# Kernel tuning notes

Measured on AMD Instinct MI355X. Metric: run time of the kernel, lower is better.

## Reference

```python
import jax, jax.numpy as jnp
import numpy as np


def _refl_conv(x, w, b, pad, stride):
    # ReflectionPad2d(pad) followed by Conv2d(stride=stride), NCHW / OIHW layouts.
    x = jnp.pad(x, ((0, 0), (0, 0), (pad, pad), (pad, pad)), mode='reflect')
    y = jax.lax.conv_general_dilated(
        x, w, window_strides=(stride, stride), padding='VALID',
        dimension_numbers=('NCHW', 'OIHW', 'NCHW'))
    return y + b[None, :, None, None]


def setup_inputs() -> dict:
    key = jax.random.key(0)
    ks = jax.random.split(key, 16)
    B, C, H, W = 8, 128, 64, 64
    IH, IW = 4 * H, 4 * W
    g = 0.02  # init gain ('normal' init in source)
    f32 = jnp.float32
    return {
        'feature_in': jax.random.normal(ks[0], (B, C, H, W), f32),
        'imgs': jax.random.uniform(ks[1], (B, 3, IH, IW), dtype=f32),
        'masks': jax.random.uniform(ks[2], (B, 1, IH, IW), dtype=f32),
        # Gate conv stack params (torch OIHW layout), biases zero per init_weights
        'gw1': g * jax.random.normal(ks[3], (32, 4, 7, 7), f32),
        'gb1': jnp.zeros((32,), f32),
        'gw2': g * jax.random.normal(ks[4], (64, 32, 5, 5), f32),
        'gb2': jnp.zeros((64,), f32),
        'gw3': g * jax.random.normal(ks[5], (128, 64, 5, 5), f32),
        'gb3': jnp.zeros((128,), f32),
        'gw4': g * jax.random.normal(ks[6], (256, 128, 3, 3), f32),
        'gb4': jnp.zeros((256,), f32),
        'gw5': g * jax.random.normal(ks[7], (1, 256, 3, 3), f32),
        'gb5': jnp.zeros((1,), f32),
        # combiner: Conv2d(2C -> C, 1x1)
        'cw': g * jax.random.normal(ks[8], (C, 2 * C, 1, 1), f32),
        'cb': jnp.zeros((C,), f32),
    }


def reference(feature_in, imgs, masks, gw1, gb1, gw2, gb2, gw3, gb3,
              gw4, gb4, gw5, gb5, cw, cb):
    PI = 3.1415926
    # ---- Gate ----
    x = jnp.concatenate([imgs, masks], axis=1)          # [B,4,4H,4W]
    s = jax.nn.relu(_refl_conv(x, gw1, gb1, 3, 1))
    s = jax.nn.relu(_refl_conv(s, gw2, gb2, 2, 2))
    s = jax.nn.relu(_refl_conv(s, gw3, gb3, 2, 1))
    s = jax.nn.relu(_refl_conv(s, gw4, gb4, 1, 2))
    s = jax.nn.relu(_refl_conv(s, gw5, gb5, 1, 1))      # [B,1,H,W]
    s = jnp.tan(PI * (jnp.tanh(s) - 0.5))
    B, C, H, W = feature_in.shape
    P = H * W
    gate = s.reshape(B, P, 1, 1)                        # row-major pixel order
    # ---- Att (patch_size=1: kernels are per-pixel feature vectors) ----
    K = feature_in.reshape(B, C, P).transpose(0, 2, 1) + 1e-7   # [B,P,C]
    Kn = K / jnp.sqrt(jnp.sum(K * K, axis=-1, keepdims=True))
    # attention_scores = conv2d(feature_map, K_norm) == cosine-like similarity
    scores = jnp.einsum('bpc,bcyx->bpyx', Kn, feature_in) + gate  # [B,P,H,W]
    A = jax.nn.softmax(scores, axis=1)
    # conv_transpose2d with 1x1 kernels == weighted sum of (unnormalized) kernels
    att = jnp.einsum('bpyx,bpc->bcyx', A, K)            # [B,C,H,W]
    # ---- combiner (1x1 conv on concat) ----
    cat = jnp.concatenate([att, feature_in], axis=1)    # [B,2C,H,W]
    out = jnp.einsum('oc,bcyx->boyx', cw[:, :, 0, 0], cat) + cb[None, :, None, None]
    return out
```

## Files before the change

### kernel.cpp

```cpp
#include <hip/hip_runtime.h>
#include <hip/hip_bf16.h>
#include <hip/hip_fp16.h>
#include <math.h>


#define PI_F 3.1415926f

typedef __attribute__((ext_vector_type(8))) short short8;
typedef __attribute__((ext_vector_type(4))) float f32x4;
typedef _Float16 half8 __attribute__((ext_vector_type(8)));
typedef __attribute__((ext_vector_type(4))) unsigned short u16x4;
typedef unsigned short ushort_t;

__device__ __forceinline__ ushort_t f2bf(float x) {
    unsigned u = __float_as_uint(x);
    unsigned r = (u + 0x7FFFu + ((u >> 16) & 1u)) >> 16;
    return (ushort_t)r;
}
__device__ __forceinline__ void split16(float x, ushort_t& h, ushort_t& l) {
    __half hh = __float2half(x);
    h = __half_as_ushort(hh);
    l = __half_as_ushort(__float2half(x - __half2float(hh)));
}
__device__ __forceinline__ ushort_t f2h(float x) {
    return __half_as_ushort(__float2half(x));
}
__device__ __forceinline__ int swz(int r, int c) {
    return ((c ^ r ^ (r >> 2)) & 3) << 3;
}

__global__ __launch_bounds__(256) void transform_w_k(
    const float* __restrict__ w, ushort_t* __restrict__ Wh, ushort_t* __restrict__ Wl,
    int Cout, int Cin, int KK)
{
    int idx = blockIdx.x * 256 + threadIdx.x;
    int N = Cout * Cin * KK;
    if (idx >= N) return;
    int oc = idx / (Cin * KK);
    int rem = idx - oc * (Cin * KK);
    int ic = rem / KK;
    int t = rem - ic * KK;
    float v = w[idx];
    long dst = ((long)t * Cout + oc) * Cin + ic;
    split16(v, Wh[dst], Wl[dst]);
}

__global__ __launch_bounds__(256) void transform_w1_k(
    const float* __restrict__ w, ushort_t* __restrict__ Wh, ushort_t* __restrict__ Wl)
{
    int idx = blockIdx.x * 256 + threadIdx.x;
    if (idx >= 7 * 32 * 32) return;
    int ky = idx / 1024;
    int rem = idx - ky * 1024;
    int oc = rem >> 5;
    int k = rem & 31;
    float v = 0.f;
    if (k < 28) {
        int kx = k >> 2, ic = k & 3;
        v = w[((oc * 4 + ic) * 7 + ky) * 7 + kx];
    }
    split16(v, Wh[idx], Wl[idx]);
}

__global__ __launch_bounds__(256) void prep_in_k(
    const float* __restrict__ imgs, const float* __restrict__ masks,
    ushort_t* __restrict__ Xh)
{
    const int iy = blockIdx.x, b = blockIdx.y;
    int sy = iy - 3; if (sy < 0) sy = -sy; if (sy >= 256) sy = 510 - sy;
    const int rb = sy << 8;
    const float* i0 = imgs + (long)b * 3 * 65536;
    const float* mk = masks + (long)b * 65536;
    for (int x = threadIdx.x; x < 262; x += 256) {
        int sx = x - 3; if (sx < 0) sx = -sx; if (sx >= 256) sx = 510 - sx;
        u16x4 hv;
        hv[0] = f2h(i0[rb + sx]);
        hv[1] = f2h(i0[65536 + rb + sx]);
        hv[2] = f2h(i0[131072 + rb + sx]);
        hv[3] = f2h(mk[rb + sx]);
        long o = ((long)(b * 262 + iy) * 262 + x) * 4;
        *(u16x4*)&Xh[o] = hv;
    }
}

__global__ __launch_bounds__(256) void conv1_mfma_k(
    const ushort_t* __restrict__ Xinh,
    const ushort_t* __restrict__ W1h, const ushort_t* __restrict__ W1l,
    const float* __restrict__ bias, ushort_t* __restrict__ Oh)
{
    const int tid = threadIdx.x, lane = tid & 63, wid = tid >> 6;
    const int wm = wid & 1, wn = wid >> 1, l15 = lane & 15, quad = lane >> 4;
    const int ox0 = blockIdx.x * 64;
    const int oy = blockIdx.y, b = blockIdx.z;
    f32x4 acc[2];
    acc[0] = (f32x4){0.f, 0.f, 0.f, 0.f};
    acc[1] = (f32x4){0.f, 0.f, 0.f, 0.f};
#pragma unroll
    for (int ky = 0; ky < 7; ++ky) {
        long wo = (long)(ky * 32 + wm * 16 + l15) * 32 + quad * 8;
        half8 Ah = *(const half8*)&W1h[wo];
        half8 Al = *(const half8*)&W1l[wo];
        long xrow = ((long)(b * 262 + oy + ky) * 262 + ox0) * 4;
#pragma unroll
        for (int ni = 0; ni < 2; ++ni) {
            long xo = xrow + (wn * 32 + ni * 16 + l15) * 4 + quad * 8;
            half8 Bh = *(const half8*)&Xinh[xo];
            acc[ni] = __builtin_amdgcn_mfma_f32_16x16x32_f16(Ah, Bh, acc[ni], 0, 0, 0);
            acc[ni] = __builtin_amdgcn_mfma_f32_16x16x32_f16(Al, Bh, acc[ni], 0, 0, 0);
        }
    }
    const int ocf = wm * 16 + quad * 4;
    float4 bv = *(const float4*)&bias[ocf];
#pragma unroll
    for (int ni = 0; ni < 2; ++ni) {
        int n = ox0 + wn * 32 + ni * 16 + l15;
        u16x4 hv;
        hv[0] = f2h(fmaxf(acc[ni][0] + bv.x, 0.f));
        hv[1] = f2h(fmaxf(acc[ni][1] + bv.y, 0.f));
        hv[2] = f2h(fmaxf(acc[ni][2] + bv.z, 0.f));
        hv[3] = f2h(fmaxf(acc[ni][3] + bv.w, 0.f));
        long o = ((long)(b * 260 + oy + 2) * 260 + n + 2) * 32 + ocf;
        *(u16x4*)&Oh[o] = hv;
    }
}

__global__ __launch_bounds__(256) void pad_cl_k(
    ushort_t* __restrict__ Xh, int Hp, int Wp, int PAD, int C, int H, int W)
{
    const int iy = blockIdx.x, b = blockIdx.y;
    int t = iy - PAD; if (t < 0) t = -t; if (t >= H) t = 2 * H - 2 - t;
    const int iys = t + PAD;
    const long rowd = ((long)(b * Hp + iy) * Wp) * C;
    const long rows = ((long)(b * Hp + iys) * Wp) * C;
    const int nch = Wp * (C >> 3);
    for (int idx = threadIdx.x; idx < nch; idx += 256) {
        int x = idx / (C >> 3);
        int cg = (idx - x * (C >> 3)) << 3;
        int t2 = x - PAD; if (t2 < 0) t2 = -t2; if (t2 >= W) t2 = 2 * W - 2 - t2;
        int xs = t2 + PAD;
        if (xs == x && iys == iy) continue;
        *(int4*)&Xh[rowd + (long)x * C + cg] = *(const int4*)&Xh[rows + (long)xs * C + cg];
    }
}

template<int K, int S, int CIN, int CSTG, int MT, int NPX, bool WRITE_CL>
__global__ __launch_bounds__(256, 2) void conv_mfma_k(
    const ushort_t* __restrict__ Xh,
    const ushort_t* __restrict__ Wh, const ushort_t* __restrict__ Wl,
    const float* __restrict__ bias,
    int Hp, int Wp, int CoutT,
    ushort_t* __restrict__ Oh, int Hpn, int Wpn, int NP,
    float* __restrict__ Ofp)
{
    constexpr int WS = (NPX - 1) * S + K;
    constexpr int WS2 = (WS + 1) / 2;
    constexpr int MF = MT / 32;
    constexpr int NF = NPX / 32;
    __shared__ ushort_t Bsh[WS * CSTG];
    __shared__ ushort_t Ash[K * MT * CSTG];
    __shared__ ushort_t Asl[K * MT * CSTG];
    const int tid = threadIdx.x, lane = tid & 63, wid = tid >> 6;
    const int wm = wid & 1, wn = wid >> 1, l15 = lane & 15, quad = lane >> 4;
    const int bx = blockIdx.x, oy = blockIdx.y;
    const int NOC = CoutT / MT;
    const int ocg = blockIdx.z % NOC, b = blockIdx.z / NOC;
    const int ox0 = bx * NPX;

    f32x4 acc[MF][NF];
#pragma unroll
    for (int mi = 0; mi < MF; ++mi)
#pragma unroll
        for (int ni = 0; ni < NF; ++ni) acc[mi][ni] = (f32x4){0.f, 0.f, 0.f, 0.f};

#pragma unroll
    for (int ky = 0; ky < K; ++ky) {
        const long rowoff = ((long)(b * Hp + oy * S + ky) * Wp + ox0 * S) * CIN;
        for (int cs = 0; cs < CIN; cs += CSTG) {
            __syncthreads();
            constexpr int NCH = WS * CSTG / 8;
#pragma unroll
            for (int it = 0; it < (NCH + 255) / 256; ++it) {
                int flat = tid + it * 256;
                if (flat < NCH) {
                    int e0 = flat * 8;
                    int x = e0 / CSTG;
                    int cpos = (e0 - x * CSTG) >> 3;
                    int xs = (S == 1) ? x : ((x >> 1) + (x & 1) * WS2);
                    *(int4*)&Bsh[xs * CSTG + swz(xs, cpos)] =
                        *(const int4*)&Xh[rowoff + (long)x * CIN + cs + cpos * 8];
                }
            }
            constexpr int NW = K * MT * CSTG / 8;
#pragma unroll
            for (int it = 0; it < (NW + 255) / 256; ++it) {
                int flat = tid + it * 256;
                if (flat < NW) {
                    int e0 = flat * 8;
                    int kx = e0 / (MT * CSTG);
                    int rem = e0 - kx * MT * CSTG;
                    int oc = rem / CSTG;
                    int cpos = (rem - oc * CSTG) >> 3;
                    int arow = kx * MT + oc;
                    int dst = arow * CSTG + swz(arow, cpos);
                    long src = ((long)((ky * K + kx) * CoutT + ocg * MT + oc)) * CIN + cs + cpos * 8;
                    *(int4*)&Ash[dst] = *(const int4*)&Wh[src];
                    *(int4*)&Asl[dst] = *(const int4*)&Wl[src];
                }
            }
            __syncthreads();
#pragma unroll
            for (int kx = 0; kx < K; ++kx) {
                half8 Ah[MF], Al[MF], Bh[NF];
#pragma unroll
                for (int mi = 0; mi < MF; ++mi) {
                    int arow = kx * MT + wm * (MT / 2) + mi * 16 + l15;
                    int ao = arow * CSTG + swz(arow, quad);
                    Ah[mi] = *(const half8*)&Ash[ao];
                    Al[mi] = *(const half8*)&Asl[ao];
                }
#pragma unroll
                for (int ni = 0; ni < NF; ++ni) {
                    int m = wn * (NPX / 2) + ni * 16 + l15;
                    int xs = (S == 1) ? (m + kx) : (m + (kx >> 1) + (kx & 1) * WS2);
                    Bh[ni] = *(const half8*)&Bsh[xs * CSTG + swz(xs, quad)];
                }
#pragma unroll
                for (int mi = 0; mi < MF; ++mi)
#pragma unroll
                    for (int ni = 0; ni < NF; ++ni) {
                        acc[mi][ni] = __builtin_amdgcn_mfma_f32_16x16x32_f16(Ah[mi], Bh[ni], acc[mi][ni], 0, 0, 0);
                        acc[mi][ni] = __builtin_amdgcn_mfma_f32_16x16x32_f16(Al[mi], Bh[ni], acc[mi][ni], 0, 0, 0);
                    }
            }
        }
    }
#pragma unroll
    for (int ni = 0; ni < NF; ++ni) {
        const int n = ox0 + wn * (NPX / 2) + ni * 16 + l15;
#pragma unroll
        for (int mi = 0; mi < MF; ++mi) {
            const int ocf = ocg * MT + wm * (MT / 2) + mi * 16 + quad * 4;
            float4 bv = *(const float4*)&bias[ocf];
            float v0 = fmaxf(acc[mi][ni][0] + bv.x, 0.f);
            float v1 = fmaxf(acc[mi][ni][1] + bv.y, 0.f);
            float v2 = fmaxf(acc[mi][ni][2] + bv.z, 0.f);
            float v3 = fmaxf(acc[mi][ni][3] + bv.w, 0.f);
            if (WRITE_CL) {
                long o = ((long)(b * Hpn + oy + NP) * Wpn + n + NP) * CoutT + ocf;
                u16x4 hv;
                hv[0] = f2h(v0); hv[1] = f2h(v1); hv[2] = f2h(v2); hv[3] = f2h(v3);
                *(u16x4*)&Oh[o] = hv;
            } else {
                long o = ((long)(b * CoutT + ocf) << 12) + (oy << 6) + n;
                Ofp[o] = v0;
                Ofp[o + 4096] = v1;
                Ofp[o + 8192] = v2;
                Ofp[o + 12288] = v3;
            }
        }
    }
}

__global__ __launch_bounds__(256) void conv5_gate_k(
    const float* __restrict__ s4, const float* __restrict__ w,
    const float* __restrict__ bias, float* __restrict__ gate)
{
    const int tid = threadIdx.x;
    const int lane = tid & 63, g = tid >> 6;
    const int oy = blockIdx.x, b = blockIdx.y;
    int ixo[3], iyo[3];
#pragma unroll
    for (int k = 0; k < 3; ++k) {
        int ix = lane + k - 1; if (ix < 0) ix = -ix; if (ix >= 64) ix = 126 - ix;
        int iy = oy + k - 1; if (iy < 0) iy = -iy; if (iy >= 64) iy = 126 - iy;
        ixo[k] = ix; iyo[k] = iy << 6;
    }
    float part = 0.f;
    const float* inb = s4 + ((long)b * 256 + g * 64) * 4096;
    const float* wg = w + g * 64 * 9;
    for (int ic = 0; ic < 64; ++ic) {
        const float* inc = inb + ic * 4096;
        const float* wc = wg + ic * 9;
#pragma unroll
        for (int ky = 0; ky < 3; ++ky)
#pragma unroll
            for (int kx = 0; kx < 3; ++kx)
                part = fmaf(wc[ky * 3 + kx], inc[iyo[ky] + ixo[kx]], part);
    }
    __shared__ float red[4][64];
    red[g][lane] = part;
    __syncthreads();
    if (tid < 64) {
        float s = bias[0] + red[0][tid] + red[1][tid] + red[2][tid] + red[3][tid];
        s = fmaxf(s, 0.f);
        gate[(b << 12) + (oy << 6) + tid] = tanf(PI_F * (tanhf(s) - 0.5f));
    }
}

__global__ __launch_bounds__(256) void invn_k(const float* __restrict__ F, float* __restrict__ invn)
{
    const int p = blockIdx.x * 256 + threadIdx.x;
    const int b = blockIdx.y;
    const float* Fb = F + (long)b * 524288;
    float ss = 0.f;
#pragma unroll 8
    for (int c = 0; c < 128; ++c) {
        float v = Fb[c * 4096 + p] + 1e-7f;
        ss = fmaf(v, v, ss);
    }
    invn[(b << 12) + p] = 1.0f / sqrtf(ss);
}

__global__ __launch_bounds__(256) void prep_bf16_k(
    const float* __restrict__ F, ushort_t* __restrict__ Fo16, ushort_t* __restrict__ Ft16)
{
    __shared__ float Ls[128][65];
    const int tid = threadIdx.x;
    const int lane = tid & 63, wv = tid >> 6;
    const int p0 = blockIdx.x * 64, b = blockIdx.y;
#pragma unroll 8
    for (int cc = 0; cc < 32; ++cc) {
        int c = wv * 32 + cc;
        long idx = ((long)b * 128 + c) * 4096 + p0 + lane;
        float v = F[idx];
        Fo16[idx] = f2bf(v);
        Ls[c][lane] = v;
    }
    __syncthreads();
#pragma unroll 8
    for (int i = 0; i < 32; ++i) {
        int flat = tid + 256 * i;
        int c = flat & 127, pl_ = flat >> 7;
        Ft16[((long)b * 4096 + p0 + pl_) * 128 + c] = f2bf(Ls[c][pl_]);
    }
}

__global__ __launch_bounds__(256) void flash_attn_k(
    const ushort_t* __restrict__ Ft16, const ushort_t* __restrict__ Fo16,
    const float* __restrict__ invn, const float* __restrict__ gate,
    float* __restrict__ Opart, float* __restrict__ lpart)
{
    __shared__ float redS[64][4];
    __shared__ ushort_t Es[2][64][72];
    const int tid = threadIdx.x, lane = tid & 63, w = tid >> 6;
    const int l15 = lane & 15, quad = lane >> 4;
    const int q0 = blockIdx.x * 64;
    const int ks = blockIdx.y, b = blockIdx.z;
    const int bp = b << 12;
    const ushort_t* Ftb = Ft16 + (long)b * 4096 * 128;
    const ushort_t* Fob = Fo16 + (long)b * 128 * 4096;

    short8 Bq[4][4];
#pragma unroll
    for (int ni = 0; ni < 4; ++ni)
#pragma unroll
        for (int cs = 0; cs < 4; ++cs)
            Bq[ni][cs] = *(const short8*)&Ftb[(long)(q0 + ni * 16 + l15) * 128 + cs * 32 + quad * 8];

    f32x4 O[2][4];
#pragma unroll
    for (int mi = 0; mi < 2; ++mi)
#pragma unroll
        for (int ni = 0; ni < 4; ++ni) O[mi][ni] = (f32x4){0.f, 0.f, 0.f, 0.f};
    float l_acc[4] = {0.f, 0.f, 0.f, 0.f};

    const int p_beg = ks * 1024;
    int buf = 0;
    for (int p0 = p_beg; p0 < p_beg + 1024; p0 += 64, buf ^= 1) {
        f32x4 Sa[4];
#pragma unroll
        for (int ni = 0; ni < 4; ++ni) Sa[ni] = (f32x4){0.f, 0.f, 0.f, 0.f};
#pragma unroll
        for (int cs = 0; cs < 4; ++cs) {
            short8 Ap = *(const short8*)&Ftb[(long)(p0 + w * 16 + l15) * 128 + cs * 32 + quad * 8];
#pragma unroll
            for (int ni = 0; ni < 4; ++ni)
                Sa[ni] = __builtin_amdgcn_mfma_f32_16x16x32_bf16(Ap, Bq[ni][cs], Sa[ni], 0, 0, 0);
        }
        float4 iv = *(const float4*)&invn[bp + p0 + w * 16 + quad * 4];
        float4 gt = *(const float4*)&gate[bp + p0 + w * 16 + quad * 4];
#pragma unroll
        for (int ni = 0; ni < 4; ++ni) {
            float e0 = __expf(fmaf(Sa[ni][0], iv.x, gt.x));
            float e1 = __expf(fmaf(Sa[ni][1], iv.y, gt.y));
            float e2 = __expf(fmaf(Sa[ni][2], iv.z, gt.z));
            float e3 = __expf(fmaf(Sa[ni][3], iv.w, gt.w));
            union { u16x4 v; __hip_bfloat162 h[2]; } u;
            u.h[0] = __float22bfloat162_rn(make_float2(e0, e1));
            u.h[1] = __float22bfloat162_rn(make_float2(e2, e3));
            *(u16x4*)&Es[buf][ni * 16 + l15][w * 16 + quad * 4] = u.v;
            l_acc[ni] += (e0 + e1) + (e2 + e3);
        }
        __syncthreads();
#pragma unroll
        for (int ksub = 0; ksub < 2; ++ksub) {
            short8 Ac[2], Be[4];
#pragma unroll
            for (int mi = 0; mi < 2; ++mi)
                Ac[mi] = *(const short8*)&Fob[(long)(w * 32 + mi * 16 + l15) * 4096 + p0 + ksub * 32 + quad * 8];
#pragma unroll
            for (int ni = 0; ni < 4; ++ni)
                Be[ni] = *(const short8*)&Es[buf][ni * 16 + l15][ksub * 32 + quad * 8];
#pragma unroll
            for (int mi = 0; mi < 2; ++mi)
#pragma unroll
                for (int ni = 0; ni < 4; ++ni)
                    O[mi][ni] = __builtin_amdgcn_mfma_f32_16x16x32_bf16(Ac[mi], Be[ni], O[mi][ni], 0, 0, 0);
        }
    }
#pragma unroll
    for (int ni = 0; ni < 4; ++ni) {
        float lt = l_acc[ni];
        lt += __shfl_xor(lt, 16);
        lt += __shfl_xor(lt, 32);
        if (quad == 0) redS[ni * 16 + l15][w] = lt;
    }
    __syncthreads();
    if (w == 0 && quad == 0) {
#pragma unroll
        for (int ni = 0; ni < 4; ++ni) {
            int q = q0 + ni * 16 + l15;
            float4 rs = *(const float4*)&redS[ni * 16 + l15][0];
            lpart[(ks * 8 + b) * 4096 + q] = (rs.x + rs.y) + (rs.z + rs.w);
        }
    }
    float* Ob = Opart + (long)(ks * 8 + b) * 524288;
#pragma unroll
    for (int mi = 0; mi < 2; ++mi)
#pragma unroll
        for (int ni = 0; ni < 4; ++ni) {
            int c = w * 32 + mi * 16 + quad * 4;
            int q = q0 + ni * 16 + l15;
#pragma unroll
            for (int r = 0; r < 4; ++r)
                Ob[((long)(c + r) << 12) + q] = O[mi][ni][r];
        }
}

__global__ __launch_bounds__(256) void combiner_k(
    const float* __restrict__ Opart, const float* __restrict__ lpart,
    const float* __restrict__ F, const float* __restrict__ cw,
    const float* __restrict__ cb, float* __restrict__ out)
{
    const int tid = threadIdx.x;
    const int q = blockIdx.x * 256 + tid;
    const int o0 = blockIdx.y << 4;
    const int b = blockIdx.z;
    float lsum = 0.f;
#pragma unroll
    for (int ks = 0; ks < 4; ++ks) lsum += lpart[(ks * 8 + b) * 4096 + q];
    float il = 1.0f / lsum;
    const float* Fb = F + (long)b * 524288 + q;
    float acc[16];
#pragma unroll
    for (int j = 0; j < 16; ++j) acc[j] = cb[o0 + j];
    for (int c = 0; c < 128; ++c) {
        float a = 0.f;
#pragma unroll
        for (int ks = 0; ks < 4; ++ks)
            a += Opart[(long)(ks * 8 + b) * 524288 + (long)c * 4096 + q];
        a *= il;
        float f = Fb[(long)c * 4096];
#pragma unroll
        for (int j = 0; j < 16; ++j) {
            acc[j] = fmaf(cw[(o0 + j) * 256 + c], a, acc[j]);
            acc[j] = fmaf(cw[(o0 + j) * 256 + 128 + c], f, acc[j]);
        }
    }
#pragma unroll
    for (int j = 0; j < 16; ++j)
        out[((long)(b * 128 + o0 + j) << 12) + q] = acc[j];
}

extern "C" void kernel_launch(void* const* d_in, const int* in_sizes, int n_in,
                              void* d_out, int out_size, void* d_ws, size_t ws_size,
                              hipStream_t stream)
{
    const float* F     = (const float*)d_in[0];
    const float* imgs  = (const float*)d_in[1];
    const float* masks = (const float*)d_in[2];
    const float* gw1 = (const float*)d_in[3];  const float* gb1 = (const float*)d_in[4];
    const float* gw2 = (const float*)d_in[5];  const float* gb2 = (const float*)d_in[6];
    const float* gw3 = (const float*)d_in[7];  const float* gb3 = (const float*)d_in[8];
    const float* gw4 = (const float*)d_in[9];  const float* gb4 = (const float*)d_in[10];
    const float* gw5 = (const float*)d_in[11]; const float* gb5 = (const float*)d_in[12];
    const float* cw  = (const float*)d_in[13]; const float* cb  = (const float*)d_in[14];
    float* out = (float*)d_out;

    float* W = (float*)d_ws;
    ushort_t* Xcl2h = (ushort_t*)(W);
    ushort_t* Xcl4h = (ushort_t*)(W);
    float*    Opart = W;
    float*    lpart = W + 16777216;
    ushort_t* Xcl3h = (ushort_t*)(W + 17305600);
    ushort_t* Fo16  = (ushort_t*)(W + 17305600);
    float*    s4   = W + 26226688;
    ushort_t* Ft16 = (ushort_t*)(W + 30420992);
    ushort_t* W2h = (ushort_t*)(W + 34615296);
    ushort_t* W2l = (ushort_t*)(W + 34640896);
    ushort_t* W3h = (ushort_t*)(W + 34666496);
    ushort_t* W3l = (ushort_t*)(W + 34768896);
    ushort_t* W4h = (ushort_t*)(W + 34871296);
    ushort_t* W4l = (ushort_t*)(W + 35018752);
    float* gate = W + 35166208;
    float* invn = W + 35198976;
    ushort_t* Xinh = (ushort_t*)(W + 35231744);
    ushort_t* W1h  = (ushort_t*)(W + 37428416);
    ushort_t* W1l  = (ushort_t*)(W + 37432000);

    transform_w_k<<<dim3(200),  256, 0, stream>>>(gw2, W2h, W2l, 64, 32, 25);
    transform_w_k<<<dim3(800),  256, 0, stream>>>(gw3, W3h, W3l, 128, 64, 25);
    transform_w_k<<<dim3(1152), 256, 0, stream>>>(gw4, W4h, W4l, 256, 128, 9);
    transform_w1_k<<<dim3(28), 256, 0, stream>>>(gw1, W1h, W1l);
    prep_in_k<<<dim3(262, 8), 256, 0, stream>>>(imgs, masks, Xinh);

    conv1_mfma_k<<<dim3(4, 256, 8), 256, 0, stream>>>(Xinh, W1h, W1l, gb1, Xcl2h);
    pad_cl_k<<<dim3(260, 8), 256, 0, stream>>>(Xcl2h, 260, 260, 2, 32, 256, 256);
    conv_mfma_k<5, 2, 32, 32, 64, 128, true><<<dim3(1, 128, 8), 256, 0, stream>>>(
        Xcl2h, W2h, W2l, gb2, 260, 260, 64, Xcl3h, 132, 132, 2, nullptr);
    pad_cl_k<<<dim3(132, 8), 256, 0, stream>>>(Xcl3h, 132, 132, 2, 64, 128, 128);
    conv_mfma_k<5, 1, 64, 32, 64, 128, true><<<dim3(1, 128, 16), 256, 0, stream>>>(
        Xcl3h, W3h, W3l, gb3, 132, 132, 128, Xcl4h, 130, 130, 1, nullptr);
    pad_cl_k<<<dim3(130, 8), 256, 0, stream>>>(Xcl4h, 130, 130, 1, 128, 128, 128);
    conv_mfma_k<3, 2, 128, 32, 128, 64, false><<<dim3(1, 64, 16), 256, 0, stream>>>(
        Xcl4h, W4h, W4l, gb4, 130, 130, 256, nullptr, 0, 0, 0, s4);
    conv5_gate_k<<<dim3(64, 8), 256, 0, stream>>>(s4, gw5, gb5, gate);

    invn_k<<<dim3(16, 8), 256, 0, stream>>>(F, invn);
    prep_bf16_k<<<dim3(64, 8), 256, 0, stream>>>(F, Fo16, Ft16);
    flash_attn_k<<<dim3(64, 4, 8), 256, 0, stream>>>(Ft16, Fo16, invn, gate, Opart, lpart);
    combiner_k<<<dim3(16, 8, 8), 256, 0, stream>>>(Opart, lpart, F, cw, cb, out);
}
```

Baseline: 667.1 us.

## Restructure flash attention so each wave owns a key slice, keeping P in registers

The attention kernel now has each of the four waves process its own 32-key slice for a 32-query tile. The S-to-P result is repacked directly into MFMA B operands in registers, which removes the shared-memory staging of exp scores and the per-iteration block barrier. The per-wave partial outputs are reduced through shared memory at the end and written out coalesced. The grid doubles, and launch bounds request three blocks per CU. The cost is a larger per-wave output accumulator (16 MFMA tiles), a serialized four-step LDS reduction, and repeated reads of V rows per wave.

```diff
diff --git a/kernel.cpp b/kernel.cpp
--- a/kernel.cpp
+++ b/kernel.cpp
@@ -335,106 +335,115 @@
     }
 }
 
-__global__ __launch_bounds__(256) void flash_attn_k(
+__global__ __launch_bounds__(256, 3) void flash_attn_k(
     const ushort_t* __restrict__ Ft16, const ushort_t* __restrict__ Fo16,
     const float* __restrict__ invn, const float* __restrict__ gate,
     float* __restrict__ Opart, float* __restrict__ lpart)
 {
-    __shared__ float redS[64][4];
-    __shared__ ushort_t Es[2][64][72];
+    __shared__ float redS[32][4];
+    __shared__ float Ored[32 * 132];
     const int tid = threadIdx.x, lane = tid & 63, w = tid >> 6;
     const int l15 = lane & 15, quad = lane >> 4;
-    const int q0 = blockIdx.x * 64;
+    const int q0 = blockIdx.x * 32;
     const int ks = blockIdx.y, b = blockIdx.z;
     const int bp = b << 12;
     const ushort_t* Ftb = Ft16 + (long)b * 4096 * 128;
     const ushort_t* Fob = Fo16 + (long)b * 128 * 4096;
 
-    short8 Bq[4][4];
-#pragma unroll
-    for (int ni = 0; ni < 4; ++ni)
+    short8 Bq[2][4];
+#pragma unroll
+    for (int ni = 0; ni < 2; ++ni)
 #pragma unroll
         for (int cs = 0; cs < 4; ++cs)
             Bq[ni][cs] = *(const short8*)&Ftb[(long)(q0 + ni * 16 + l15) * 128 + cs * 32 + quad * 8];
 
-    f32x4 O[2][4];
-#pragma unroll
-    for (int mi = 0; mi < 2; ++mi)
-#pragma unroll
-        for (int ni = 0; ni < 4; ++ni) O[mi][ni] = (f32x4){0.f, 0.f, 0.f, 0.f};
-    float l_acc[4] = {0.f, 0.f, 0.f, 0.f};
-
+    f32x4 O[2][8];
+#pragma unroll
+    for (int ni = 0; ni < 2; ++ni)
+#pragma unroll
+        for (int ct = 0; ct < 8; ++ct) O[ni][ct] = (f32x4){0.f, 0.f, 0.f, 0.f};
+    float l_acc[2] = {0.f, 0.f};
+
+    union BeU { short8 v; __hip_bfloat162 h[4]; };
     const int p_beg = ks * 1024;
-    int buf = 0;
-    for (int p0 = p_beg; p0 < p_beg + 1024; p0 += 64, buf ^= 1) {
-        f32x4 Sa[4];
-#pragma unroll
-        for (int ni = 0; ni < 4; ++ni) Sa[ni] = (f32x4){0.f, 0.f, 0.f, 0.f};
-#pragma unroll
-        for (int cs = 0; cs < 4; ++cs) {
-            short8 Ap = *(const short8*)&Ftb[(long)(p0 + w * 16 + l15) * 128 + cs * 32 + quad * 8];
-#pragma unroll
-            for (int ni = 0; ni < 4; ++ni)
-                Sa[ni] = __builtin_amdgcn_mfma_f32_16x16x32_bf16(Ap, Bq[ni][cs], Sa[ni], 0, 0, 0);
-        }
-        float4 iv = *(const float4*)&invn[bp + p0 + w * 16 + quad * 4];
-        float4 gt = *(const float4*)&gate[bp + p0 + w * 16 + quad * 4];
-#pragma unroll
-        for (int ni = 0; ni < 4; ++ni) {
-            float e0 = __expf(fmaf(Sa[ni][0], iv.x, gt.x));
-            float e1 = __expf(fmaf(Sa[ni][1], iv.y, gt.y));
-            float e2 = __expf(fmaf(Sa[ni][2], iv.z, gt.z));
-            float e3 = __expf(fmaf(Sa[ni][3], iv.w, gt.w));
-            union { u16x4 v; __hip_bfloat162 h[2]; } u;
-            u.h[0] = __float22bfloat162_rn(make_float2(e0, e1));
-            u.h[1] = __float22bfloat162_rn(make_float2(e2, e3));
-            *(u16x4*)&Es[buf][ni * 16 + l15][w * 16 + quad * 4] = u.v;
-            l_acc[ni] += (e0 + e1) + (e2 + e3);
-        }
-        __syncthreads();
-#pragma unroll
-        for (int ksub = 0; ksub < 2; ++ksub) {
-            short8 Ac[2], Be[4];
-#pragma unroll
-            for (int mi = 0; mi < 2; ++mi)
-                Ac[mi] = *(const short8*)&Fob[(long)(w * 32 + mi * 16 + l15) * 4096 + p0 + ksub * 32 + quad * 8];
-#pragma unroll
-            for (int ni = 0; ni < 4; ++ni)
-                Be[ni] = *(const short8*)&Es[buf][ni * 16 + l15][ksub * 32 + quad * 8];
-#pragma unroll
-            for (int mi = 0; mi < 2; ++mi)
-#pragma unroll
-                for (int ni = 0; ni < 4; ++ni)
-                    O[mi][ni] = __builtin_amdgcn_mfma_f32_16x16x32_bf16(Ac[mi], Be[ni], O[mi][ni], 0, 0, 0);
-        }
-    }
-#pragma unroll
-    for (int ni = 0; ni < 4; ++ni) {
+    const int prow_base = ((l15 & 12) << 1) + (l15 & 3);
+
+    for (int t = 0; t < 8; ++t) {
+        const int p0w = p_beg + t * 128 + w * 32;
+        BeU be0, be1;
+#pragma unroll
+        for (int sub = 0; sub < 2; ++sub) {
+            const long prow = p0w + prow_base + sub * 4;
+            f32x4 Sa[2];
+            Sa[0] = (f32x4){0.f, 0.f, 0.f, 0.f};
+            Sa[1] = (f32x4){0.f, 0.f, 0.f, 0.f};
+#pragma unroll
+            for (int cs = 0; cs < 4; ++cs) {
+                short8 Ap = *(const short8*)&Ftb[prow * 128 + cs * 32 + quad * 8];
+                Sa[0] = __builtin_amdgcn_mfma_f32_16x16x32_bf16(Ap, Bq[0][cs], Sa[0], 0, 0, 0);
+                Sa[1] = __builtin_amdgcn_mfma_f32_16x16x32_bf16(Ap, Bq[1][cs], Sa[1], 0, 0, 0);
+            }
+            float4 iv = *(const float4*)&invn[bp + p0w + quad * 8 + sub * 4];
+            float4 gt = *(const float4*)&gate[bp + p0w + quad * 8 + sub * 4];
+#pragma unroll
+            for (int ni = 0; ni < 2; ++ni) {
+                float e0 = __expf(fmaf(Sa[ni][0], iv.x, gt.x));
+                float e1 = __expf(fmaf(Sa[ni][1], iv.y, gt.y));
+                float e2 = __expf(fmaf(Sa[ni][2], iv.z, gt.z));
+                float e3 = __expf(fmaf(Sa[ni][3], iv.w, gt.w));
+                BeU& be = (ni == 0) ? be0 : be1;
+                be.h[sub * 2]     = __float22bfloat162_rn(make_float2(e0, e1));
+                be.h[sub * 2 + 1] = __float22bfloat162_rn(make_float2(e2, e3));
+                l_acc[ni] += (e0 + e1) + (e2 + e3);
+            }
+        }
+#pragma unroll
+        for (int ct = 0; ct < 8; ++ct) {
+            short8 Va = *(const short8*)&Fob[(long)(ct * 16 + l15) * 4096 + p0w + quad * 8];
+            O[0][ct] = __builtin_amdgcn_mfma_f32_16x16x32_bf16(Va, be0.v, O[0][ct], 0, 0, 0);
+            O[1][ct] = __builtin_amdgcn_mfma_f32_16x16x32_bf16(Va, be1.v, O[1][ct], 0, 0, 0);
+        }
+    }
+
+#pragma unroll
+    for (int ni = 0; ni < 2; ++ni) {
         float lt = l_acc[ni];
         lt += __shfl_xor(lt, 16);
         lt += __shfl_xor(lt, 32);
         if (quad == 0) redS[ni * 16 + l15][w] = lt;
     }
     __syncthreads();
-    if (w == 0 && quad == 0) {
-#pragma unroll
-        for (int ni = 0; ni < 4; ++ni) {
-            int q = q0 + ni * 16 + l15;
-            float4 rs = *(const float4*)&redS[ni * 16 + l15][0];
-            lpart[(ks * 8 + b) * 4096 + q] = (rs.x + rs.y) + (rs.z + rs.w);
-        }
+
+#pragma unroll
+    for (int rw = 0; rw < 4; ++rw) {
+        if (w == rw) {
+#pragma unroll
+            for (int ni = 0; ni < 2; ++ni)
+#pragma unroll
+                for (int ct = 0; ct < 8; ++ct) {
+                    float* dst = &Ored[(ni * 16 + l15) * 132 + ct * 16 + quad * 4];
+                    if (rw == 0) {
+                        *(float4*)dst = make_float4(O[ni][ct][0], O[ni][ct][1], O[ni][ct][2], O[ni][ct][3]);
+                    } else {
+                        float4 v = *(const float4*)dst;
+                        v.x += O[ni][ct][0]; v.y += O[ni][ct][1];
+                        v.z += O[ni][ct][2]; v.w += O[ni][ct][3];
+                        *(float4*)dst = v;
+                    }
+                }
+        }
+        __syncthreads();
+    }
+
+    if (tid < 32) {
+        float4 rs = *(const float4*)&redS[tid][0];
+        lpart[(ks * 8 + b) * 4096 + q0 + tid] = (rs.x + rs.y) + (rs.z + rs.w);
     }
     float* Ob = Opart + (long)(ks * 8 + b) * 524288;
-#pragma unroll
-    for (int mi = 0; mi < 2; ++mi)
-#pragma unroll
-        for (int ni = 0; ni < 4; ++ni) {
-            int c = w * 32 + mi * 16 + quad * 4;
-            int q = q0 + ni * 16 + l15;
-#pragma unroll
-            for (int r = 0; r < 4; ++r)
-                Ob[((long)(c + r) << 12) + q] = O[mi][ni][r];
-        }
+    const int qw = tid & 31, cg = (tid >> 5) * 16;
+#pragma unroll
+    for (int j = 0; j < 16; ++j)
+        Ob[((long)(cg + j) << 12) + q0 + qw] = Ored[qw * 132 + cg + j];
 }
 
 __global__ __launch_bounds__(256) void combiner_k(
@@ -528,6 +537,6 @@
 
     invn_k<<<dim3(16, 8), 256, 0, stream>>>(F, invn);
     prep_bf16_k<<<dim3(64, 8), 256, 0, stream>>>(F, Fo16, Ft16);
-    flash_attn_k<<<dim3(64, 4, 8), 256, 0, stream>>>(Ft16, Fo16, invn, gate, Opart, lpart);
+    flash_attn_k<<<dim3(128, 4, 8), 256, 0, stream>>>(Ft16, Fo16, invn, gate, Opart, lpart);
     combiner_k<<<dim3(16, 8, 8), 256, 0, stream>>>(Opart, lpart, F, cw, cb, out);
 }
```

Result: slower. 829.5 us (+24.3%).

## Restructure flash attention into single-wave blocks with register-resident P tiles

Applied to the files above, without the earlier changes.

Each flash-attention block is now a single 64-thread wavefront that handles all 128 channels of the output for its 64 queries. The row permutation of the score MFMA is arranged so the exp'd bf16 scores land directly in the B-operand register layout of the second MFMA. This removes the LDS staging buffer and the per-iteration __syncthreads. In exchange each wave holds 128 f32 accumulators, which raises register pressure, and occupancy drops to one wave per block. The block count rises to 2048, and B-tile loads are no longer shared across waves.

```diff
diff --git a/kernel.cpp b/kernel.cpp
--- a/kernel.cpp
+++ b/kernel.cpp
@@ -335,17 +335,16 @@
     }
 }
 
-__global__ __launch_bounds__(256) void flash_attn_k(
+__global__ __launch_bounds__(64, 1) void flash_attn_k(
     const ushort_t* __restrict__ Ft16, const ushort_t* __restrict__ Fo16,
     const float* __restrict__ invn, const float* __restrict__ gate,
     float* __restrict__ Opart, float* __restrict__ lpart)
 {
-    __shared__ float redS[64][4];
-    __shared__ ushort_t Es[2][64][72];
-    const int tid = threadIdx.x, lane = tid & 63, w = tid >> 6;
+    const int lane = threadIdx.x & 63;
     const int l15 = lane & 15, quad = lane >> 4;
-    const int q0 = blockIdx.x * 64;
-    const int ks = blockIdx.y, b = blockIdx.z;
+    const int b = blockIdx.x;
+    const int qb = blockIdx.y & 63, ks = blockIdx.y >> 6;
+    const int q0 = qb * 64;
     const int bp = b << 12;
     const ushort_t* Ftb = Ft16 + (long)b * 4096 * 128;
     const ushort_t* Fob = Fo16 + (long)b * 128 * 4096;
@@ -357,83 +356,73 @@
         for (int cs = 0; cs < 4; ++cs)
             Bq[ni][cs] = *(const short8*)&Ftb[(long)(q0 + ni * 16 + l15) * 128 + cs * 32 + quad * 8];
 
-    f32x4 O[2][4];
-#pragma unroll
-    for (int mi = 0; mi < 2; ++mi)
-#pragma unroll
-        for (int ni = 0; ni < 4; ++ni) O[mi][ni] = (f32x4){0.f, 0.f, 0.f, 0.f};
+    f32x4 O[8][4];
+#pragma unroll
+    for (int ct = 0; ct < 8; ++ct)
+#pragma unroll
+        for (int ni = 0; ni < 4; ++ni) O[ct][ni] = (f32x4){0.f, 0.f, 0.f, 0.f};
     float l_acc[4] = {0.f, 0.f, 0.f, 0.f};
 
+    union BeU { short8 v; __hip_bfloat162 h[4]; };
     const int p_beg = ks * 1024;
-    int buf = 0;
-    for (int p0 = p_beg; p0 < p_beg + 1024; p0 += 64, buf ^= 1) {
-        f32x4 Sa[4];
-#pragma unroll
-        for (int ni = 0; ni < 4; ++ni) Sa[ni] = (f32x4){0.f, 0.f, 0.f, 0.f};
-#pragma unroll
-        for (int cs = 0; cs < 4; ++cs) {
-            short8 Ap = *(const short8*)&Ftb[(long)(p0 + w * 16 + l15) * 128 + cs * 32 + quad * 8];
+    const int prow_base = ((l15 & 12) << 1) + (l15 & 3);
+
+    for (int t = 0; t < 32; ++t) {
+        const int p0w = p_beg + t * 32;
+        BeU be[4];
+#pragma unroll
+        for (int sub = 0; sub < 2; ++sub) {
+            const long prow = p0w + prow_base + sub * 4;
+            f32x4 Sa[4];
+#pragma unroll
+            for (int ni = 0; ni < 4; ++ni) Sa[ni] = (f32x4){0.f, 0.f, 0.f, 0.f};
+#pragma unroll
+            for (int cs = 0; cs < 4; ++cs) {
+                short8 Ap = *(const short8*)&Ftb[prow * 128 + cs * 32 + quad * 8];
+#pragma unroll
+                for (int ni = 0; ni < 4; ++ni)
+                    Sa[ni] = __builtin_amdgcn_mfma_f32_16x16x32_bf16(Ap, Bq[ni][cs], Sa[ni], 0, 0, 0);
+            }
+            float4 iv = *(const float4*)&invn[bp + p0w + quad * 8 + sub * 4];
+            float4 gt = *(const float4*)&gate[bp + p0w + quad * 8 + sub * 4];
+#pragma unroll
+            for (int ni = 0; ni < 4; ++ni) {
+                float e0 = __expf(fmaf(Sa[ni][0], iv.x, gt.x));
+                float e1 = __expf(fmaf(Sa[ni][1], iv.y, gt.y));
+                float e2 = __expf(fmaf(Sa[ni][2], iv.z, gt.z));
+                float e3 = __expf(fmaf(Sa[ni][3], iv.w, gt.w));
+                be[ni].h[sub * 2]     = __float22bfloat162_rn(make_float2(e0, e1));
+                be[ni].h[sub * 2 + 1] = __float22bfloat162_rn(make_float2(e2, e3));
+                l_acc[ni] += (e0 + e1) + (e2 + e3);
+            }
+        }
+#pragma unroll
+        for (int ct = 0; ct < 8; ++ct) {
+            short8 Va = *(const short8*)&Fob[(long)(ct * 16 + l15) * 4096 + p0w + quad * 8];
 #pragma unroll
             for (int ni = 0; ni < 4; ++ni)
-                Sa[ni] = __builtin_amdgcn_mfma_f32_16x16x32_bf16(Ap, Bq[ni][cs], Sa[ni], 0, 0, 0);
-        }
-        float4 iv = *(const float4*)&invn[bp + p0 + w * 16 + quad * 4];
-        float4 gt = *(const float4*)&gate[bp + p0 + w * 16 + quad * 4];
-#pragma unroll
-        for (int ni = 0; ni < 4; ++ni) {
-            float e0 = __expf(fmaf(Sa[ni][0], iv.x, gt.x));
-            float e1 = __expf(fmaf(Sa[ni][1], iv.y, gt.y));
-            float e2 = __expf(fmaf(Sa[ni][2], iv.z, gt.z));
-            float e3 = __expf(fmaf(Sa[ni][3], iv.w, gt.w));
-            union { u16x4 v; __hip_bfloat162 h[2]; } u;
-            u.h[0] = __float22bfloat162_rn(make_float2(e0, e1));
-            u.h[1] = __float22bfloat162_rn(make_float2(e2, e3));
-            *(u16x4*)&Es[buf][ni * 16 + l15][w * 16 + quad * 4] = u.v;
-            l_acc[ni] += (e0 + e1) + (e2 + e3);
-        }
-        __syncthreads();
-#pragma unroll
-        for (int ksub = 0; ksub < 2; ++ksub) {
-            short8 Ac[2], Be[4];
-#pragma unroll
-            for (int mi = 0; mi < 2; ++mi)
-                Ac[mi] = *(const short8*)&Fob[(long)(w * 32 + mi * 16 + l15) * 4096 + p0 + ksub * 32 + quad * 8];
-#pragma unroll
-            for (int ni = 0; ni < 4; ++ni)
-                Be[ni] = *(const short8*)&Es[buf][ni * 16 + l15][ksub * 32 + quad * 8];
-#pragma unroll
-            for (int mi = 0; mi < 2; ++mi)
-#pragma unroll
-                for (int ni = 0; ni < 4; ++ni)
-                    O[mi][ni] = __builtin_amdgcn_mfma_f32_16x16x32_bf16(Ac[mi], Be[ni], O[mi][ni], 0, 0, 0);
-        }
-    }
+                O[ct][ni] = __builtin_amdgcn_mfma_f32_16x16x32_bf16(Va, be[ni].v, O[ct][ni], 0, 0, 0);
+        }
+    }
+
 #pragma unroll
     for (int ni = 0; ni < 4; ++ni) {
         float lt = l_acc[ni];
         lt += __shfl_xor(lt, 16);
         lt += __shfl_xor(lt, 32);
-        if (quad == 0) redS[ni * 16 + l15][w] = lt;
-    }
-    __syncthreads();
-    if (w == 0 && quad == 0) {
+        if (quad == 0)
+            lpart[(ks * 8 + b) * 4096 + q0 + ni * 16 + l15] = lt;
+    }
+    float* Ob = Opart + (long)(ks * 8 + b) * 524288;
+#pragma unroll
+    for (int ct = 0; ct < 8; ++ct)
 #pragma unroll
         for (int ni = 0; ni < 4; ++ni) {
+            int c = ct * 16 + quad * 4;
             int q = q0 + ni * 16 + l15;
-            float4 rs = *(const float4*)&redS[ni * 16 + l15][0];
-            lpart[(ks * 8 + b) * 4096 + q] = (rs.x + rs.y) + (rs.z + rs.w);
-        }
-    }
-    float* Ob = Opart + (long)(ks * 8 + b) * 524288;
-#pragma unroll
-    for (int mi = 0; mi < 2; ++mi)
-#pragma unroll
-        for (int ni = 0; ni < 4; ++ni) {
-            int c = w * 32 + mi * 16 + quad * 4;
-            int q = q0 + ni * 16 + l15;
 #pragma unroll
             for (int r = 0; r < 4; ++r)
-                Ob[((long)(c + r) << 12) + q] = O[mi][ni][r];
+                Ob[((long)(c + r) << 12) + q] = O[ct][ni][r];
         }
 }
 
@@ -528,6 +517,6 @@
 
     invn_k<<<dim3(16, 8), 256, 0, stream>>>(F, invn);
     prep_bf16_k<<<dim3(64, 8), 256, 0, stream>>>(F, Fo16, Ft16);
-    flash_attn_k<<<dim3(64, 4, 8), 256, 0, stream>>>(Ft16, Fo16, invn, gate, Opart, lpart);
+    flash_attn_k<<<dim3(8, 256, 1), 64, 0, stream>>>(Ft16, Fo16, invn, gate, Opart, lpart);
     combiner_k<<<dim3(16, 8, 8), 256, 0, stream>>>(Opart, lpart, F, cw, cb, out);
 }
```

New measurement: 644.9 us. 3.3% less time.
